# Performance work log

Hardware: AMD Instinct MI355X
Metric: run time of the kernel (lower is better)

Reference implementation:

```python
import jax, jax.numpy as jnp
import numpy as np

N_NODES = 100000

def _sage(x, src, tgt, Wl, bl, Wr):
    # PyG SAGEConv (mean aggr): out = lin_l(mean_{j in N(i)} x_j) + lin_r(x_i)
    msg = x[src]                                             # [E, F] gather
    s = jax.ops.segment_sum(msg, tgt, num_segments=N_NODES)  # [N, F]
    cnt = jax.ops.segment_sum(jnp.ones((src.shape[0], 1), x.dtype), tgt, num_segments=N_NODES)
    agg = s / jnp.maximum(cnt, 1.0)
    return agg @ Wl + bl + x @ Wr


def setup_inputs() -> dict:
    key = jax.random.key(0)
    ks = jax.random.split(key, 16)
    node_dim, edge_dim, hidden = 128, 16, 64
    E = 1000000
    x = jax.random.normal(ks[0], (N_NODES, node_dim), jnp.float32)
    edge_index = jax.random.randint(ks[1], (2, E), 0, N_NODES, jnp.int64)
    edge_attr = jax.random.normal(ks[2], (E, edge_dim), jnp.float32)
    def lin(k, fi, fo, scale=None):
        s = scale if scale is not None else 1.0 / np.sqrt(fi)
        return jax.random.uniform(k, (fi, fo), jnp.float32, -s, s)
    return {
        "x": x, "edge_index": edge_index, "edge_attr": edge_attr,
        # edge MLP: Linear(16,64) -> ReLU -> Linear(64,64)
        "We1": lin(ks[3], edge_dim, hidden), "be1": jnp.zeros((hidden,), jnp.float32),
        "We2": lin(ks[4], hidden, hidden),   "be2": jnp.zeros((hidden,), jnp.float32),
        # SAGEConv 0: lin_l (with bias, on aggregated) + lin_r (no bias, on root)
        "Wl0": lin(ks[5], node_dim, hidden), "bl0": jnp.zeros((hidden,), jnp.float32),
        "Wr0": lin(ks[6], node_dim, hidden),
        # SAGEConv 1
        "Wl1": lin(ks[7], hidden, hidden), "bl1": jnp.zeros((hidden,), jnp.float32),
        "Wr1": lin(ks[8], hidden, hidden),
        # output MLP: Linear(64,64) -> ReLU -> (Dropout eval=id) -> Linear(64,1)
        "Wo1": lin(ks[9], hidden, hidden), "bo1": jnp.zeros((hidden,), jnp.float32),
        "Wo2": lin(ks[10], hidden, 1),     "bo2": jnp.zeros((1,), jnp.float32),
    }


def reference(x, edge_index, edge_attr, We1, be1, We2, be2,
              Wl0, bl0, Wr0, Wl1, bl1, Wr1, Wo1, bo1, Wo2, bo2):
    src, tgt = edge_index[0], edge_index[1]
    # edge MLP (dropout in eval mode = identity)
    ea = jax.nn.relu(edge_attr @ We1 + be1) @ We2 + be2       # [E, H]
    # two SAGE layers with ReLU
    h = jax.nn.relu(_sage(x, src, tgt, Wl0, bl0, Wr0))        # [N, H]
    h = jax.nn.relu(_sage(h, src, tgt, Wl1, bl1, Wr1))        # [N, H]
    # per-edge features: gather both endpoints + edge embedding
    ef = h[src] + h[tgt] + ea                                 # [E, H]
    out = jax.nn.relu(ef @ Wo1 + bo1) @ Wo2 + bo2             # [E, 1]
    return jax.nn.sigmoid(out[:, 0])                          # [E]
```

## Files before the change

### kernel.cpp

```cpp
#include <hip/hip_runtime.h>
#include <math.h>

typedef __attribute__((ext_vector_type(8))) short short8;
typedef __attribute__((ext_vector_type(4))) float f32x4;

#define CAPB 4096

static __device__ __forceinline__ unsigned short f2bf(float f) {
  union { float f; unsigned int u; } x; x.f = f;
  unsigned int r = x.u + 0x7fffu + ((x.u >> 16) & 1u);
  return (unsigned short)(r >> 16);
}
static __device__ __forceinline__ float bf2f(unsigned int u) {
  union { unsigned int u; float f; } x; x.u = u << 16; return x.f;
}

__global__ void k_flag(const unsigned int* __restrict__ w, int nSample,
                       unsigned int* __restrict__ flag,
                       int* __restrict__ gcursor) {
  if (blockIdx.x == 1) {
    if (threadIdx.x < 256) { gcursor[threadIdx.x] = 0; gcursor[threadIdx.x + 256] = 0; }
    return;
  }
  if (blockIdx.x != 0) return;
  __shared__ unsigned int red[256];
  unsigned int v = 0;
  for (int i = threadIdx.x; i < nSample; i += 256) v |= w[2 * i + 1];
  red[threadIdx.x] = v;
  __syncthreads();
  for (int s = 128; s > 0; s >>= 1) {
    if (threadIdx.x < s) red[threadIdx.x] |= red[threadIdx.x + s];
    __syncthreads();
  }
  if (threadIdx.x == 0) flag[0] = red[0];
}

template <int K, bool BF16IN, int NTILES, bool INLINEW>
__device__ __forceinline__ void ngemm_body(
    const void* __restrict__ Xv, const unsigned short* __restrict__ WnT,
    const float* __restrict__ W0f, const float* __restrict__ W1f,
    unsigned short* __restrict__ Y0, unsigned short* __restrict__ Y1,
    int N, int blk, unsigned short* __restrict__ sX) {
  constexpr int STR = K + 8;
  constexpr int NC = K / 32;
  const int tid = threadIdx.x;
  const int wv = tid >> 6, lane = tid & 63;
  const int m = lane & 15, q = lane >> 4;
  const int row0 = blk * 64;

  short8 bB[NTILES][NC];
#pragma unroll
  for (int ct = 0; ct < NTILES; ++ct)
#pragma unroll
    for (int c = 0; c < NC; ++c) {
      if constexpr (INLINEW) {
        int n = (NTILES == 2) ? (wv * 32 + ct * 16 + m) : (wv * 16 + m);
        const float* Wf = (n < 64) ? W0f : W1f;
        int nn = n & 63;
        union { short8 s; unsigned short h[8]; } ub;
#pragma unroll
        for (int j = 0; j < 8; ++j)
          ub.h[j] = f2bf(Wf[(size_t)(c * 32 + q * 8 + j) * 64 + nn]);
        bB[ct][c] = ub.s;
      } else {
        int n = (NTILES == 2) ? (wv * 32 + ct * 16 + m) : (wv * 16 + m);
        bB[ct][c] = *(const short8*)(WnT + (size_t)n * K + c * 32 + q * 8);
      }
    }

#pragma unroll
  for (int i = 0; i < K / 16; ++i) {
    int f = tid + 256 * i;
    int r = f / (K / 4);
    int c4 = f % (K / 4);
    int rr = row0 + r; if (rr >= N) rr = N - 1;
    uint2 pk;
    if constexpr (BF16IN) {
      pk = *(const uint2*)((const unsigned short*)Xv + (size_t)rr * K + c4 * 4);
    } else {
      float4 v = *(const float4*)((const float*)Xv + (size_t)rr * K + c4 * 4);
      pk.x = (unsigned int)f2bf(v.x) | ((unsigned int)f2bf(v.y) << 16);
      pk.y = (unsigned int)f2bf(v.z) | ((unsigned int)f2bf(v.w) << 16);
    }
    *(uint2*)(sX + r * STR + c4 * 4) = pk;
  }
  __syncthreads();

  f32x4 acc[4][NTILES];
#pragma unroll
  for (int rt = 0; rt < 4; ++rt)
#pragma unroll
    for (int ct = 0; ct < NTILES; ++ct)
#pragma unroll
      for (int r = 0; r < 4; ++r) acc[rt][ct][r] = 0.f;

#pragma unroll
  for (int c = 0; c < NC; ++c) {
    short8 a[4];
#pragma unroll
    for (int rt = 0; rt < 4; ++rt)
      a[rt] = *(const short8*)(sX + (rt * 16 + m) * STR + c * 32 + q * 8);
#pragma unroll
    for (int rt = 0; rt < 4; ++rt)
#pragma unroll
      for (int ct = 0; ct < NTILES; ++ct)
        acc[rt][ct] = __builtin_amdgcn_mfma_f32_16x16x32_bf16(a[rt], bB[ct][c], acc[rt][ct], 0, 0, 0);
  }

#pragma unroll
  for (int rt = 0; rt < 4; ++rt)
#pragma unroll
    for (int ct = 0; ct < NTILES; ++ct) {
      unsigned short* Yw;
      int n;
      if constexpr (NTILES == 2) {
        Yw = (wv < 2) ? Y0 : Y1;
        n = (wv & 1) * 32 + ct * 16 + m;
      } else {
        Yw = Y0;
        n = wv * 16 + m;
      }
#pragma unroll
      for (int reg = 0; reg < 4; ++reg) {
        int row = row0 + rt * 16 + q * 4 + reg;
        if (row < N) Yw[(size_t)row * 64 + n] = f2bf(acc[rt][ct][reg]);
      }
    }
}

template <int K, bool BF16IN, int NTILES>
__global__ __launch_bounds__(256) void k_ngemm(
    const void* __restrict__ Xv, const unsigned short* __restrict__ WnT,
    unsigned short* __restrict__ Y0, unsigned short* __restrict__ Y1, int N) {
  __shared__ __align__(16) unsigned short sX[64 * (K + 8)];
  ngemm_body<K, BF16IN, NTILES, false>(Xv, WnT, nullptr, nullptr, Y0, Y1, N,
                                       blockIdx.x, sX);
}

__global__ __launch_bounds__(256) void k_mega1(
    const unsigned int* __restrict__ w, const unsigned int* __restrict__ flag,
    int E, int nDec, int nWork, int gB,
    int* __restrict__ src, int* __restrict__ tgt,
    int* __restrict__ gcursor, unsigned int* __restrict__ tmp,
    const float* __restrict__ x, unsigned short* __restrict__ Yl,
    unsigned short* __restrict__ Yr, int N,
    const float* __restrict__ We2, const float* __restrict__ Wo1,
    const float* __restrict__ be2, const float* __restrict__ bo1,
    const float* __restrict__ We1,
    const float* __restrict__ Wl0, const float* __restrict__ Wr0,
    const float* __restrict__ Wl1, const float* __restrict__ Wr1,
    unsigned short* __restrict__ W25T, unsigned short* __restrict__ We1T,
    unsigned short* __restrict__ Wo1T, float* __restrict__ cvec,
    unsigned short* __restrict__ WnT1) {
  __shared__ __align__(16) char smem[64 * 136 * 2];
  const int tid = threadIdx.x;
  const int tot = nDec + nWork;
  const int di  = (int)(((long long)blockIdx.x * nDec) / tot);
  const int di1 = (int)(((long long)(blockIdx.x + 1) * nDec) / tot);

  if (di1 > di) {
    int* hist = (int*)smem;
    hist[tid] = 0; hist[tid + 256] = 0;
    __syncthreads();
    const int e0 = di * 4096;
    const int e1 = (e0 + 4096 < E) ? (e0 + 4096) : E;
    const unsigned int fl = flag[0];
    for (int e = e0 + tid; e < e1; e += 256) {
      int s, t;
      if (fl) { s = (int)w[e]; t = (int)w[E + e]; }
      else    { s = (int)w[2 * e]; t = (int)w[2 * (E + e)]; }
      src[e] = s; tgt[e] = t;
      atomicAdd(hist + (t >> 8), 1);
    }
    __syncthreads();
    {
      int c0 = hist[tid], c1 = hist[tid + 256];
      int s0 = (c0 > 0) ? atomicAdd(gcursor + tid, c0) : 0;
      int s1 = (c1 > 0) ? atomicAdd(gcursor + tid + 256, c1) : 0;
      __syncthreads();
      hist[tid] = s0; hist[tid + 256] = s1;
    }
    __syncthreads();
    for (int e = e0 + tid; e < e1; e += 256) {
      int s, t;
      if (fl) { s = (int)w[e]; t = (int)w[E + e]; }
      else    { s = (int)w[2 * e]; t = (int)w[2 * (E + e)]; }
      int b = t >> 8;
      int pos = atomicAdd(hist + b, 1);
      if (pos < CAPB)
        tmp[(size_t)b * CAPB + pos] = ((unsigned int)s << 8) | (unsigned int)(t & 255);
    }
    return;
  }
  const int wi = blockIdx.x - di;
  if (wi == 0) {
    float* sB = (float*)smem;
    for (int i = tid; i < 1024; i += 256)
      *(float4*)&sB[i * 4] = *(const float4*)(Wo1 + i * 4);
    __syncthreads();
    for (int idx = tid; idx < 4096; idx += 256) {
      int k = idx >> 6, n = idx & 63;
      float s = 0.f;
#pragma unroll 8
      for (int mm = 0; mm < 64; ++mm) s = fmaf(We2[k * 64 + mm], sB[mm * 64 + n], s);
      W25T[n * 64 + k] = f2bf(s);
      Wo1T[n * 64 + k] = f2bf(sB[k * 64 + n]);
    }
    for (int idx = tid; idx < 2048; idx += 256) {
      int n = idx >> 5, k = idx & 31;
      We1T[n * 32 + k] = (k < 16) ? f2bf(We1[k * 64 + n]) : (unsigned short)0;
    }
    if (tid < 64) {
      float s = bo1[tid];
#pragma unroll 8
      for (int mm = 0; mm < 64; ++mm) s = fmaf(be2[mm], sB[mm * 64 + tid], s);
      cvec[tid] = s;
    }
  } else if (wi <= 32) {
    int idx = (wi - 1) * 256 + tid;
    int n = idx >> 6, k = idx & 63;
    float v = (n < 64) ? Wl1[(size_t)k * 64 + n] : Wr1[(size_t)k * 64 + (n - 64)];
    WnT1[idx] = f2bf(v);
  } else {
    ngemm_body<128, false, 2, true>(x, nullptr, Wl0, Wr0, Yl, Yr, N,
                                    wi - 33, (unsigned short*)smem);
  }
}

__global__ __launch_bounds__(256) void k_bsort(
    const unsigned int* __restrict__ tmp, const int* __restrict__ gcursor,
    int* __restrict__ csrc, uint2* __restrict__ rowptr2, int N, int nBuck,
    const float4* __restrict__ ef, uint2* __restrict__ eb, int nItems) {
  __shared__ int cnt[256];
  __shared__ int curs[256];
  __shared__ int wsum[4];
  const int tid = threadIdx.x;
  if (blockIdx.x >= nBuck) {
    const int ci = blockIdx.x - nBuck;
#pragma unroll
    for (int j = 0; j < 4; ++j) {
      int i = ci * 1024 + j * 256 + tid;
      if (i < nItems) {
        float4 v = ef[i];
        uint2 pk;
        pk.x = (unsigned int)f2bf(v.x) | ((unsigned int)f2bf(v.y) << 16);
        pk.y = (unsigned int)f2bf(v.z) | ((unsigned int)f2bf(v.w) << 16);
        eb[i] = pk;
      }
    }
    return;
  }
  const int b = blockIdx.x;
  int c = gcursor[b]; if (c > CAPB) c = CAPB;
  cnt[tid] = 0;
  __syncthreads();
  const unsigned int* reg = tmp + (size_t)b * CAPB;
  for (int i = tid; i < c; i += 256) atomicAdd(&cnt[reg[i] & 255u], 1);
  __syncthreads();
  const int lane = tid & 63, wv = tid >> 6;
  int v = cnt[tid];
  int incl = v;
#pragma unroll
  for (int off = 1; off < 64; off <<= 1) {
    int t = __shfl_up(incl, off, 64);
    if (lane >= off) incl += t;
  }
  if (lane == 63) wsum[wv] = incl;
  __syncthreads();
  int add = 0;
  for (int ww = 0; ww < wv; ++ww) add += wsum[ww];
  int excl = add + incl - v;
  curs[tid] = excl;
  int node = b * 256 + tid;
  if (node < N)
    rowptr2[node] = make_uint2((unsigned int)(b * CAPB + excl),
                               (unsigned int)(b * CAPB + excl + v));
  __syncthreads();
  for (int i = tid; i < c; i += 256) {
    unsigned int wd = reg[i];
    int p = atomicAdd(&curs[wd & 255u], 1);
    csrc[(size_t)b * CAPB + p] = (int)(wd >> 8);
  }
}

__global__ __launch_bounds__(256) void k_agg(
    const unsigned short* __restrict__ Y, const uint2* __restrict__ rowptr2,
    const int* __restrict__ csrc, const float* __restrict__ bias,
    const unsigned short* __restrict__ Yr, unsigned short* __restrict__ H,
    int N) {
  int node = (blockIdx.x * 256 + threadIdx.x) >> 6;
  if (node >= N) return;
  const int lane = threadIdx.x & 63;
  const int c4 = lane & 15, rr = lane >> 4;
  uint2 be = rowptr2[node];
  int beg = (int)be.x, end = (int)be.y;
  float a0 = 0.f, a1 = 0.f, a2 = 0.f, a3 = 0.f;
  float b0 = 0.f, b1 = 0.f, b2 = 0.f, b3 = 0.f;
  for (int e = beg; e < end; e += 8) {
    int e0 = e + rr, e1 = e + 4 + rr;
    if (e0 < end) {
      int s = csrc[e0];
      uint2 v = *(const uint2*)(Y + (size_t)s * 64 + c4 * 4);
      a0 += bf2f(v.x & 0xffffu); a1 += bf2f(v.x >> 16);
      a2 += bf2f(v.y & 0xffffu); a3 += bf2f(v.y >> 16);
    }
    if (e1 < end) {
      int s = csrc[e1];
      uint2 v = *(const uint2*)(Y + (size_t)s * 64 + c4 * 4);
      b0 += bf2f(v.x & 0xffffu); b1 += bf2f(v.x >> 16);
      b2 += bf2f(v.y & 0xffffu); b3 += bf2f(v.y >> 16);
    }
  }
  a0 += b0; a1 += b1; a2 += b2; a3 += b3;
#pragma unroll
  for (int msk = 16; msk <= 32; msk <<= 1) {
    a0 += __shfl_xor(a0, msk, 64);
    a1 += __shfl_xor(a1, msk, 64);
    a2 += __shfl_xor(a2, msk, 64);
    a3 += __shfl_xor(a3, msk, 64);
  }
  if (rr == 0) {
    float cdeg = (float)(end - beg);
    if (cdeg < 1.f) cdeg = 1.f;
    float inv = 1.f / cdeg;
    float4 bv = *(const float4*)(bias + c4 * 4);
    uint2 yv = *(const uint2*)(Yr + (size_t)node * 64 + c4 * 4);
    float o0 = fmaxf(a0 * inv + bv.x + bf2f(yv.x & 0xffffu), 0.f);
    float o1 = fmaxf(a1 * inv + bv.y + bf2f(yv.x >> 16), 0.f);
    float o2 = fmaxf(a2 * inv + bv.z + bf2f(yv.y & 0xffffu), 0.f);
    float o3 = fmaxf(a3 * inv + bv.w + bf2f(yv.y >> 16), 0.f);
    uint2 pk;
    pk.x = (unsigned int)f2bf(o0) | ((unsigned int)f2bf(o1) << 16);
    pk.y = (unsigned int)f2bf(o2) | ((unsigned int)f2bf(o3) << 16);
    *(uint2*)(H + (size_t)node * 64 + c4 * 4) = pk;
  }
}

#define T1_STRIDE 72
#define G_STRIDE 68
__global__ __launch_bounds__(256) void k_edge3(
    const unsigned short* __restrict__ EAb, const int* __restrict__ src,
    const int* __restrict__ tgt, const unsigned short* __restrict__ Gb,
    const unsigned short* __restrict__ We1T,
    const unsigned short* __restrict__ W25T,
    const float* __restrict__ cvec, const float* __restrict__ be1,
    const float* __restrict__ Wo2, const float* __restrict__ bo2,
    float* __restrict__ out, int E, int nT, int nWaves) {
  __shared__ unsigned short sT1a[4][16 * T1_STRIDE];
  __shared__ float sGa[4][16 * G_STRIDE];
  const int tid = threadIdx.x;
  const int wid = tid >> 6, lane = tid & 63;
  const int m = lane & 15, q = lane >> 4;
  unsigned short* sT1 = sT1a[wid];
  float* sG = sGa[wid];

  short8 bWe1[4], bW25[4][2];
  float cv[4], wo2v[4], be1v[4];
#pragma unroll
  for (int nt = 0; nt < 4; ++nt) {
    int n = nt * 16 + m;
    bWe1[nt] = *(const short8*)(We1T + n * 32 + q * 8);
    bW25[nt][0] = *(const short8*)(W25T + n * 64 + q * 8);
    bW25[nt][1] = *(const short8*)(W25T + n * 64 + 32 + q * 8);
    cv[nt] = cvec[n];
    wo2v[nt] = Wo2[n];
    be1v[nt] = be1[n];
  }
  const float b_out = bo2[0];
  const short8 zfrag = {};

  int t = blockIdx.x * 4 + wid;
  if (t >= nT) return;
  int il = t * 16 + m; if (il >= E) il = E - 1;
  int my_idx = (lane < 16) ? src[il] : ((lane < 32) ? tgt[il] : 0);

  while (true) {
    const int base = t * 16;
    const int tn = t + nWaves;
    const bool last = (tn >= nT);
    const int tc = last ? t : tn;

    int il_n = tc * 16 + m; if (il_n >= E) il_n = E - 1;
    int idx_n = (lane < 16) ? src[il_n] : ((lane < 32) ? tgt[il_n] : 0);

    int rs[4], rt[4];
#pragma unroll
    for (int r = 0; r < 4; ++r) {
      rs[r] = __shfl(my_idx, q * 4 + r, 64);
      rt[r] = __shfl(my_idx, 16 + q * 4 + r, 64);
    }
    uint2 sv[4], tv[4];
#pragma unroll
    for (int r = 0; r < 4; ++r) {
      sv[r] = *(const uint2*)(Gb + (size_t)rs[r] * 64 + m * 4);
      tv[r] = *(const uint2*)(Gb + (size_t)rt[r] * 64 + m * 4);
    }

    int er = base + m; if (er >= E) er = E - 1;
    short8 aEA = zfrag;
    if (q < 2) aEA = *(const short8*)(EAb + (size_t)er * 16 + (q & 1) * 8);

    f32x4 t1[4];
#pragma unroll
    for (int nt = 0; nt < 4; ++nt) {
      f32x4 cinit; cinit[0] = be1v[nt]; cinit[1] = be1v[nt];
      cinit[2] = be1v[nt]; cinit[3] = be1v[nt];
      t1[nt] = __builtin_amdgcn_mfma_f32_16x16x32_bf16(aEA, bWe1[nt], cinit, 0, 0, 0);
    }
#pragma unroll
    for (int nt = 0; nt < 4; ++nt)
#pragma unroll
      for (int r = 0; r < 4; ++r)
        sT1[(q * 4 + r) * T1_STRIDE + nt * 16 + m] = f2bf(fmaxf(t1[nt][r], 0.f));
    short8 aT0 = *(short8*)(sT1 + m * T1_STRIDE + q * 8);
    short8 aT1 = *(short8*)(sT1 + m * T1_STRIDE + 32 + q * 8);

#pragma unroll
    for (int r = 0; r < 4; ++r) {
      f32x4 g;
      g[0] = bf2f(sv[r].x & 0xffffu) + bf2f(tv[r].x & 0xffffu);
      g[1] = bf2f(sv[r].x >> 16)     + bf2f(tv[r].x >> 16);
      g[2] = bf2f(sv[r].y & 0xffffu) + bf2f(tv[r].y & 0xffffu);
      g[3] = bf2f(sv[r].y >> 16)     + bf2f(tv[r].y >> 16);
      *(f32x4*)(sG + (q * 4 + r) * G_STRIDE + m * 4) = g;
    }

    f32x4 acc[4];
#pragma unroll
    for (int nt = 0; nt < 4; ++nt)
#pragma unroll
      for (int r = 0; r < 4; ++r)
        acc[nt][r] = cv[nt] + sG[(q * 4 + r) * G_STRIDE + nt * 16 + m];
#pragma unroll
    for (int nt = 0; nt < 4; ++nt) {
      acc[nt] = __builtin_amdgcn_mfma_f32_16x16x32_bf16(aT0, bW25[nt][0], acc[nt], 0, 0, 0);
      acc[nt] = __builtin_amdgcn_mfma_f32_16x16x32_bf16(aT1, bW25[nt][1], acc[nt], 0, 0, 0);
    }

    float p[4];
#pragma unroll
    for (int r = 0; r < 4; ++r) {
      p[r] = fmaxf(acc[0][r], 0.f) * wo2v[0] + fmaxf(acc[1][r], 0.f) * wo2v[1] +
             fmaxf(acc[2][r], 0.f) * wo2v[2] + fmaxf(acc[3][r], 0.f) * wo2v[3];
    }
#pragma unroll
    for (int msk = 1; msk <= 8; msk <<= 1) {
#pragma unroll
      for (int r = 0; r < 4; ++r) p[r] += __shfl_xor(p[r], msk, 64);
    }
    if (m == 0) {
#pragma unroll
      for (int r = 0; r < 4; ++r) {
        int row = base + q * 4 + r;
        if (row < E) out[row] = 1.f / (1.f + __expf(-(p[r] + b_out)));
      }
    }

    if (last) break;
    t = tn; my_idx = idx_n;
  }
}

extern "C" void kernel_launch(void* const* d_in, const int* in_sizes, int n_in,
                              void* d_out, int out_size, void* d_ws, size_t ws_size,
                              hipStream_t stream) {
  const float* x     = (const float*)d_in[0];
  const unsigned int* eidx = (const unsigned int*)d_in[1];
  const float* eattr = (const float*)d_in[2];
  const float* We1 = (const float*)d_in[3];
  const float* be1 = (const float*)d_in[4];
  const float* We2 = (const float*)d_in[5];
  const float* be2 = (const float*)d_in[6];
  const float* Wl0 = (const float*)d_in[7];
  const float* bl0 = (const float*)d_in[8];
  const float* Wr0 = (const float*)d_in[9];
  const float* Wl1 = (const float*)d_in[10];
  const float* bl1 = (const float*)d_in[11];
  const float* Wr1 = (const float*)d_in[12];
  const float* Wo1 = (const float*)d_in[13];
  const float* bo1 = (const float*)d_in[14];
  const float* Wo2 = (const float*)d_in[15];
  const float* bo2 = (const float*)d_in[16];

  const int N = in_sizes[0] / 128;
  const int E = in_sizes[2] / 16;
  const int NBUCK = (N + 255) >> 8;
  float* out = (float*)d_out;

  char* ws = (char*)d_ws;
  size_t off = 0;
  auto alloc = [&](size_t bytes) {
    char* p = ws + off;
    off += (bytes + 255) & ~(size_t)255;
    return p;
  };
  unsigned int* flag = (unsigned int*)alloc(256);
  int* src    = (int*)alloc((size_t)E * 4);
  int* tgt    = (int*)alloc((size_t)E * 4);
  int* gcursor = (int*)alloc(512 * 4);
  unsigned int* tmp = (unsigned int*)alloc((size_t)NBUCK * CAPB * 4);
  int* csrc   = (int*)alloc((size_t)NBUCK * CAPB * 4);
  uint2* rowptr2 = (uint2*)alloc((size_t)N * 8);
  unsigned short* EAb = (unsigned short*)alloc((size_t)E * 16 * 2);
  unsigned short* Hb = (unsigned short*)alloc((size_t)N * 64 * 2);
  unsigned short* Yl = (unsigned short*)alloc((size_t)N * 64 * 2);
  unsigned short* Yr = (unsigned short*)alloc((size_t)N * 64 * 2);
  unsigned short* Gb = (unsigned short*)alloc((size_t)N * 64 * 2);
  unsigned short* W25T = (unsigned short*)alloc(64 * 64 * 2);
  unsigned short* We1T = (unsigned short*)alloc(64 * 32 * 2);
  unsigned short* Wo1T = (unsigned short*)alloc(64 * 64 * 2);
  unsigned short* WnT1 = (unsigned short*)alloc(128 * 64 * 2);
  float* cvec = (float*)alloc(64 * 4);
  (void)ws_size; (void)n_in; (void)out_size;

  k_flag<<<2, 256, 0, stream>>>(eidx, 8192, flag, gcursor);

  const int nDec = (E + 4095) / 4096;
  const int gB = (N + 63) / 64;
  const int nWork = 33 + gB;
  k_mega1<<<nDec + nWork, 256, 0, stream>>>(
      eidx, flag, E, nDec, nWork, gB,
      src, tgt, gcursor, tmp,
      x, Yl, Yr, N,
      We2, Wo1, be2, bo1, We1, Wl0, Wr0, Wl1, Wr1,
      W25T, We1T, Wo1T, cvec, WnT1);

  const int nConv = (E * 4 + 1023) / 1024;
  k_bsort<<<NBUCK + nConv, 256, 0, stream>>>(tmp, gcursor, csrc, rowptr2, N,
                                             NBUCK, (const float4*)eattr,
                                             (uint2*)EAb, E * 4);

  const int aggB = (N + 3) / 4;
  k_agg<<<aggB, 256, 0, stream>>>(Yl, rowptr2, csrc, bl0, Yr, Hb, N);

  k_ngemm<64, true, 2><<<gB, 256, 0, stream>>>(Hb, WnT1, Yl, Yr, N);
  k_agg<<<aggB, 256, 0, stream>>>(Yl, rowptr2, csrc, bl1, Yr, Hb, N);

  k_ngemm<64, true, 1><<<gB, 256, 0, stream>>>(Hb, Wo1T, Gb, nullptr, N);

  const int nT = (E + 15) / 16;
  const int blocks = 3072;
  k_edge3<<<blocks, 256, 0, stream>>>(EAb, src, tgt, Gb, We1T, W25T, cvec,
                                      be1, Wo2, bo2, out, E, nT, blocks * 4);
}
```

Before: 401.5 us.

## Aggregate before transform in layer 2 and fuse SAGE GEMM with output GEMM

Layer 2 now mean-aggregates the raw layer-1 hidden features first, instead of transforming them and then aggregating. A single fused kernel then concatenates the aggregate with the root features, applies the combined [Wl1;Wr1] weight plus bias and ReLU, and immediately multiplies by Wo1, keeping the intermediate in shared memory. This removes one launch and the global round trip of Yl/Yr and the layer-2 hidden state. It adds an extra N×64 buffer, and the gather in the second aggregation reads the same 64-wide bf16 rows as before.

Result: faster. 386.6 us (-3.7%).

```diff
diff --git a/kernel.cpp b/kernel.cpp
--- a/kernel.cpp
+++ b/kernel.cpp
@@ -126,15 +126,6 @@
         if (row < N) Yw[(size_t)row * 64 + n] = f2bf(acc[rt][ct][reg]);
       }
     }
-}
-
-template <int K, bool BF16IN, int NTILES>
-__global__ __launch_bounds__(256) void k_ngemm(
-    const void* __restrict__ Xv, const unsigned short* __restrict__ WnT,
-    unsigned short* __restrict__ Y0, unsigned short* __restrict__ Y1, int N) {
-  __shared__ __align__(16) unsigned short sX[64 * (K + 8)];
-  ngemm_body<K, BF16IN, NTILES, false>(Xv, WnT, nullptr, nullptr, Y0, Y1, N,
-                                       blockIdx.x, sX);
 }
 
 __global__ __launch_bounds__(256) void k_mega1(
@@ -151,7 +142,7 @@
     const float* __restrict__ Wl1, const float* __restrict__ Wr1,
     unsigned short* __restrict__ W25T, unsigned short* __restrict__ We1T,
     unsigned short* __restrict__ Wo1T, float* __restrict__ cvec,
-    unsigned short* __restrict__ WnT1) {
+    unsigned short* __restrict__ WnL2T) {
   __shared__ __align__(16) char smem[64 * 136 * 2];
   const int tid = threadIdx.x;
   const int tot = nDec + nWork;
@@ -218,9 +209,10 @@
     }
   } else if (wi <= 32) {
     int idx = (wi - 1) * 256 + tid;
-    int n = idx >> 6, k = idx & 63;
-    float v = (n < 64) ? Wl1[(size_t)k * 64 + n] : Wr1[(size_t)k * 64 + (n - 64)];
-    WnT1[idx] = f2bf(v);
+    int n = idx >> 7, k = idx & 127;
+    float v = (k < 64) ? Wl1[(size_t)k * 64 + n]
+                       : Wr1[(size_t)(k - 64) * 64 + n];
+    WnL2T[idx] = f2bf(v);
   } else {
     ngemm_body<128, false, 2, true>(x, nullptr, Wl0, Wr0, Yl, Yr, N,
                                     wi - 33, (unsigned short*)smem);
@@ -283,6 +275,7 @@
   }
 }
 
+template <bool RAW>
 __global__ __launch_bounds__(256) void k_agg(
     const unsigned short* __restrict__ Y, const uint2* __restrict__ rowptr2,
     const int* __restrict__ csrc, const float* __restrict__ bias,
@@ -323,17 +316,99 @@
     float cdeg = (float)(end - beg);
     if (cdeg < 1.f) cdeg = 1.f;
     float inv = 1.f / cdeg;
-    float4 bv = *(const float4*)(bias + c4 * 4);
-    uint2 yv = *(const uint2*)(Yr + (size_t)node * 64 + c4 * 4);
-    float o0 = fmaxf(a0 * inv + bv.x + bf2f(yv.x & 0xffffu), 0.f);
-    float o1 = fmaxf(a1 * inv + bv.y + bf2f(yv.x >> 16), 0.f);
-    float o2 = fmaxf(a2 * inv + bv.z + bf2f(yv.y & 0xffffu), 0.f);
-    float o3 = fmaxf(a3 * inv + bv.w + bf2f(yv.y >> 16), 0.f);
+    float o0, o1, o2, o3;
+    if constexpr (RAW) {
+      o0 = a0 * inv; o1 = a1 * inv; o2 = a2 * inv; o3 = a3 * inv;
+    } else {
+      float4 bv = *(const float4*)(bias + c4 * 4);
+      uint2 yv = *(const uint2*)(Yr + (size_t)node * 64 + c4 * 4);
+      o0 = fmaxf(a0 * inv + bv.x + bf2f(yv.x & 0xffffu), 0.f);
+      o1 = fmaxf(a1 * inv + bv.y + bf2f(yv.x >> 16), 0.f);
+      o2 = fmaxf(a2 * inv + bv.z + bf2f(yv.y & 0xffffu), 0.f);
+      o3 = fmaxf(a3 * inv + bv.w + bf2f(yv.y >> 16), 0.f);
+    }
     uint2 pk;
     pk.x = (unsigned int)f2bf(o0) | ((unsigned int)f2bf(o1) << 16);
     pk.y = (unsigned int)f2bf(o2) | ((unsigned int)f2bf(o3) << 16);
     *(uint2*)(H + (size_t)node * 64 + c4 * 4) = pk;
   }
+}
+
+__global__ __launch_bounds__(256) void k_gemm2g(
+    const unsigned short* __restrict__ A1, const unsigned short* __restrict__ H,
+    const float* __restrict__ bl1, const unsigned short* __restrict__ WnL2T,
+    const unsigned short* __restrict__ Wo1T, unsigned short* __restrict__ Gb,
+    int N) {
+  __shared__ __align__(16) unsigned short sX[64 * 136];
+  __shared__ __align__(16) unsigned short sH2[64 * 72];
+  const int tid = threadIdx.x;
+  const int wv = tid >> 6, lane = tid & 63;
+  const int m = lane & 15, q = lane >> 4;
+  const int row0 = blockIdx.x * 64;
+  const int n = wv * 16 + m;
+
+  short8 bB1[4], bB2[2];
+#pragma unroll
+  for (int c = 0; c < 4; ++c)
+    bB1[c] = *(const short8*)(WnL2T + (size_t)n * 128 + c * 32 + q * 8);
+#pragma unroll
+  for (int c = 0; c < 2; ++c)
+    bB2[c] = *(const short8*)(Wo1T + (size_t)n * 64 + c * 32 + q * 8);
+  const float bl = bl1[n];
+
+#pragma unroll
+  for (int i = 0; i < 8; ++i) {
+    int f = tid + 256 * i;
+    int r = f >> 5;
+    int c4 = f & 31;
+    int rr = row0 + r; if (rr >= N) rr = N - 1;
+    uint2 pk;
+    if (c4 < 16) pk = *(const uint2*)(A1 + (size_t)rr * 64 + c4 * 4);
+    else         pk = *(const uint2*)(H  + (size_t)rr * 64 + (c4 - 16) * 4);
+    *(uint2*)(sX + r * 136 + c4 * 4) = pk;
+  }
+  __syncthreads();
+
+  f32x4 acc[4];
+#pragma unroll
+  for (int rt = 0; rt < 4; ++rt)
+#pragma unroll
+    for (int r = 0; r < 4; ++r) acc[rt][r] = 0.f;
+#pragma unroll
+  for (int c = 0; c < 4; ++c)
+#pragma unroll
+    for (int rt = 0; rt < 4; ++rt) {
+      short8 a = *(const short8*)(sX + (rt * 16 + m) * 136 + c * 32 + q * 8);
+      acc[rt] = __builtin_amdgcn_mfma_f32_16x16x32_bf16(a, bB1[c], acc[rt], 0, 0, 0);
+    }
+
+#pragma unroll
+  for (int rt = 0; rt < 4; ++rt)
+#pragma unroll
+    for (int reg = 0; reg < 4; ++reg)
+      sH2[(rt * 16 + q * 4 + reg) * 72 + n] = f2bf(fmaxf(acc[rt][reg] + bl, 0.f));
+  __syncthreads();
+
+  f32x4 acc2[4];
+#pragma unroll
+  for (int rt = 0; rt < 4; ++rt)
+#pragma unroll
+    for (int r = 0; r < 4; ++r) acc2[rt][r] = 0.f;
+#pragma unroll
+  for (int c = 0; c < 2; ++c)
+#pragma unroll
+    for (int rt = 0; rt < 4; ++rt) {
+      short8 a = *(const short8*)(sH2 + (rt * 16 + m) * 72 + c * 32 + q * 8);
+      acc2[rt] = __builtin_amdgcn_mfma_f32_16x16x32_bf16(a, bB2[c], acc2[rt], 0, 0, 0);
+    }
+
+#pragma unroll
+  for (int rt = 0; rt < 4; ++rt)
+#pragma unroll
+    for (int reg = 0; reg < 4; ++reg) {
+      int row = row0 + rt * 16 + q * 4 + reg;
+      if (row < N) Gb[(size_t)row * 64 + n] = f2bf(acc2[rt][reg]);
+    }
 }
 
 #define T1_STRIDE 72
@@ -503,13 +578,14 @@
   uint2* rowptr2 = (uint2*)alloc((size_t)N * 8);
   unsigned short* EAb = (unsigned short*)alloc((size_t)E * 16 * 2);
   unsigned short* Hb = (unsigned short*)alloc((size_t)N * 64 * 2);
+  unsigned short* A1 = (unsigned short*)alloc((size_t)N * 64 * 2);
   unsigned short* Yl = (unsigned short*)alloc((size_t)N * 64 * 2);
   unsigned short* Yr = (unsigned short*)alloc((size_t)N * 64 * 2);
   unsigned short* Gb = (unsigned short*)alloc((size_t)N * 64 * 2);
   unsigned short* W25T = (unsigned short*)alloc(64 * 64 * 2);
   unsigned short* We1T = (unsigned short*)alloc(64 * 32 * 2);
   unsigned short* Wo1T = (unsigned short*)alloc(64 * 64 * 2);
-  unsigned short* WnT1 = (unsigned short*)alloc(128 * 64 * 2);
+  unsigned short* WnL2T = (unsigned short*)alloc(64 * 128 * 2);
   float* cvec = (float*)alloc(64 * 4);
   (void)ws_size; (void)n_in; (void)out_size;
 
@@ -523,7 +599,7 @@
       src, tgt, gcursor, tmp,
       x, Yl, Yr, N,
       We2, Wo1, be2, bo1, We1, Wl0, Wr0, Wl1, Wr1,
-      W25T, We1T, Wo1T, cvec, WnT1);
+      W25T, We1T, Wo1T, cvec, WnL2T);
 
   const int nConv = (E * 4 + 1023) / 1024;
   k_bsort<<<NBUCK + nConv, 256, 0, stream>>>(tmp, gcursor, csrc, rowptr2, N,
@@ -531,12 +607,10 @@
                                              (uint2*)EAb, E * 4);
 
   const int aggB = (N + 3) / 4;
-  k_agg<<<aggB, 256, 0, stream>>>(Yl, rowptr2, csrc, bl0, Yr, Hb, N);
-
-  k_ngemm<64, true, 2><<<gB, 256, 0, stream>>>(Hb, WnT1, Yl, Yr, N);
-  k_agg<<<aggB, 256, 0, stream>>>(Yl, rowptr2, csrc, bl1, Yr, Hb, N);
-
-  k_ngemm<64, true, 1><<<gB, 256, 0, stream>>>(Hb, Wo1T, Gb, nullptr, N);
+  k_agg<false><<<aggB, 256, 0, stream>>>(Yl, rowptr2, csrc, bl0, Yr, Hb, N);
+  k_agg<true><<<aggB, 256, 0, stream>>>(Hb, rowptr2, csrc, nullptr, nullptr,
+                                        A1, N);
+  k_gemm2g<<<gB, 256, 0, stream>>>(A1, Hb, bl1, WnL2T, Wo1T, Gb, N);
 
   const int nT = (E + 15) / 16;
   const int blocks = 3072;
```
